# Optimization experiments

Hardware: AMD Instinct MI355X
Metric: run time of the kernel (lower is better)

The kernel has to match this reference:

```python
import jax, jax.numpy as jnp
import numpy as np

# Production-scale dims inferred from graph_construct / coord_cuda:
# coord_cuda: [batch, total_len, mat_h*mat_w, edge_num, 2]
B, T, C, H, W, K = 4, 8, 32, 40, 40, 9
EPS = 1e-8


def setup_inputs() -> dict:
    key = jax.random.key(0)
    sim_feat = jax.random.normal(key, (B, T, C, H, W), dtype=jnp.float32)
    return {"sim_feat": sim_feat}


def reference(sim_feat):
    """Motion-graph construction: similarity matrix between consecutive
    frames' node features, kNN edge selection (top edge_num), per-node
    edge weight normalization, and coordinate-displacement node init."""
    b, t, c, h, w = sim_feat.shape
    hw = h * w
    # [B, T, hw, c] node features
    feat = sim_feat.reshape(b, t, c, hw).transpose(0, 1, 3, 2)
    # cosine-style normalization for the similarity matrix
    fn = feat * jax.lax.rsqrt(jnp.sum(feat * feat, axis=-1, keepdims=True) + EPS)
    # build_similarity_matrix ('forward'): frame t nodes vs frame t+1 nodes
    # sim: [B, T-1, hw, hw] -- dominant, memory-bound intermediate
    sim = jnp.einsum('btic,btjc->btij', fn[:, :-1], fn[:, 1:])
    # build_graph_edge: top edge_num candidate edges per source node
    wgt, idx = jax.lax.top_k(sim, K)          # [B, T-1, hw, K]
    # edge_normalize: weights sum to 1 over the K edges of each node
    wgt = wgt / (jnp.sum(wgt, axis=-1, keepdims=True) + EPS)
    # target node 2D coords (y, x) via gather on flat index
    ty = idx // w
    tx = idx % w
    # source node coords (motion_node_indices analogue)
    src = jnp.arange(hw, dtype=idx.dtype)
    sy = (src // w)[None, None, :, None]
    sx = (src % w)[None, None, :, None]
    # node_init = target coord - source coord (motion displacement), [B,T-1,hw,K,2]
    node_init = jnp.stack([ty - sy, tx - sx], axis=-1)
    return wgt, idx, node_init
```

## Files before the change

kernel.cpp:

```cpp
#include <hip/hip_runtime.h>
#include <math.h>

#define BD   4
#define TD   8
#define CD   32
#define WD   40
#define KD   9
#define HWD  1600
#define TM1  7
#define NPAIR (BD * TM1)
#define OUTK ((size_t)NPAIR * HWD * KD)
#define CL   6
#define NEX  12

#define FNW_OFF   0
#define TRAW_OFF  3276800
#define RND_OFF   9830400

typedef __attribute__((ext_vector_type(8))) short short8;
typedef __attribute__((ext_vector_type(4))) float f32x4;

__device__ __forceinline__ uint f2bf(float f) {
    uint u = __float_as_uint(f);
    return (u + 0x7FFFu + ((u >> 16) & 1u)) >> 16;
}

__global__ __launch_bounds__(256)
void prep_kernel(const float* __restrict__ x, uint* __restrict__ fnw,
                 float* __restrict__ traw, double* __restrict__ rnd)
{
    const int gid  = blockIdx.x * 256 + threadIdx.x;
    const int q    = gid & 3;
    const int idx  = gid >> 2;
    const int bt   = idx / HWD;
    const int node = idx - bt * HWD;

    const float* src = x + (size_t)bt * CD * HWD + node;
    float v[8];
    float ssq = 0.f;
    double ssd = 0.0;
#pragma unroll
    for (int cc = 0; cc < 8; ++cc) {
        const float a = src[(size_t)(q * 8 + cc) * HWD];
        v[cc] = a;
        ssq += a * a;
        ssd = fma((double)a, (double)a, ssd);
    }
    ssq += __shfl_xor(ssq, 1);  ssq += __shfl_xor(ssq, 2);
    ssd += __shfl_xor(ssd, 1);  ssd += __shfl_xor(ssd, 2);

    const float rn = 1.0f / sqrtf(ssq + 1e-8f);
    if (q == 0) rnd[(size_t)bt * HWD + node] = 1.0 / sqrt(ssd + 1e-8);

    uint* dstb = fnw + (size_t)(bt * HWD + node) * 16 + q * 4;
    const uint w0 = f2bf(v[0]*rn) | (f2bf(v[1]*rn) << 16);
    const uint w1 = f2bf(v[2]*rn) | (f2bf(v[3]*rn) << 16);
    const uint w2 = f2bf(v[4]*rn) | (f2bf(v[5]*rn) << 16);
    const uint w3 = f2bf(v[6]*rn) | (f2bf(v[7]*rn) << 16);
    *(uint4*)dstb = make_uint4(w0, w1, w2, w3);

    float* dstr = traw + (size_t)(bt * HWD + node) * 32 + q * 8;
    ((float4*)dstr)[0] = make_float4(v[0], v[1], v[2], v[3]);
    ((float4*)dstr)[1] = make_float4(v[4], v[5], v[6], v[7]);
}

__global__ __launch_bounds__(256)
void topk_kernel(const uint* __restrict__ fnw, const float* __restrict__ traw,
                 const double* __restrict__ rnd, float* __restrict__ out)
{
    __shared__ uint s_ext[2][64][NEX];

    const int tid  = threadIdx.x;
    const int lane = tid & 63;
    const int wid  = tid >> 6;
    const int li   = lane & 15;
    const int gr   = lane >> 4;
    const int iq   = wid & 1;
    const int half = wid >> 1;

    const int bid  = blockIdx.x;
    const int xcd  = bid & 7;
    const int kk   = bid >> 3;
    const int work = xcd * 175 + kk;
    const int f    = work / 50;
    const int rem  = work - f * 50;
    const int b    = f / TM1;
    const int t    = f - b * TM1;
    const int bt0  = b * TD + t;
    const int bt1  = bt0 + 1;
    const int i    = rem * 32 + iq * 16 + li;

    const uint* fA = fnw + (size_t)bt0 * HWD * 16;
    const uint* fB = fnw + (size_t)bt1 * HWD * 16;

    const short8 bF = *(const short8*)(fA + (size_t)i * 16 + gr * 4);

    uint C[4][CL];
#pragma unroll
    for (int r = 0; r < 4; ++r)
#pragma unroll
        for (int k = 0; k < CL; ++k) C[r][k] = 0u;

    int jr[4];
#pragma unroll
    for (int r = 0; r < 4; ++r) jr[r] = 2047 - half * 800 - 4 * gr - r;

    const f32x4 one4 = {1.f, 1.f, 1.f, 1.f};

#define LDT(dst, s) dst = *(const short8*)(fB + (size_t)((s) * 16 + li) * 16 + gr * 4)

#define INSTILE(acc) do {                                              \
    _Pragma("unroll")                                                  \
    for (int r = 0; r < 4; ++r) {                                      \
        int ub = __float_as_int((acc)[r]);                             \
        ub = ub < 0 ? 0 : ub;                                          \
        uint u = ((uint)ub & 0xFFFFF800u) | (uint)jr[r];               \
        uint tv = u;                                                   \
        _Pragma("unroll")                                              \
        for (int k = 0; k < CL; ++k) {                                 \
            const uint lo = min(C[r][k], tv);                          \
            C[r][k] = max(C[r][k], tv);                                \
            tv = lo;                                                   \
        }                                                              \
        jr[r] -= 16;                                                   \
    }                                                                  \
} while (0)

    const int s0 = half * 50;
    short8 a0, a1, a2, a3;
    LDT(a0, s0); LDT(a1, s0 + 1); LDT(a2, s0 + 2); LDT(a3, s0 + 3);

    for (int sb = s0; sb < s0 + 44; sb += 4) {
        f32x4 acc;
        acc = __builtin_amdgcn_mfma_f32_16x16x32_bf16(a0, bF, one4, 0, 0, 0);
        LDT(a0, sb + 4);
        INSTILE(acc);
        acc = __builtin_amdgcn_mfma_f32_16x16x32_bf16(a1, bF, one4, 0, 0, 0);
        LDT(a1, sb + 5);
        INSTILE(acc);
        acc = __builtin_amdgcn_mfma_f32_16x16x32_bf16(a2, bF, one4, 0, 0, 0);
        LDT(a2, sb + 6);
        INSTILE(acc);
        acc = __builtin_amdgcn_mfma_f32_16x16x32_bf16(a3, bF, one4, 0, 0, 0);
        LDT(a3, sb + 7);
        INSTILE(acc);
    }
    {
        f32x4 acc;
        acc = __builtin_amdgcn_mfma_f32_16x16x32_bf16(a0, bF, one4, 0, 0, 0);
        LDT(a0, s0 + 48);
        INSTILE(acc);
        acc = __builtin_amdgcn_mfma_f32_16x16x32_bf16(a1, bF, one4, 0, 0, 0);
        LDT(a1, s0 + 49);
        INSTILE(acc);
        acc = __builtin_amdgcn_mfma_f32_16x16x32_bf16(a2, bF, one4, 0, 0, 0);
        INSTILE(acc);
        acc = __builtin_amdgcn_mfma_f32_16x16x32_bf16(a3, bF, one4, 0, 0, 0);
        INSTILE(acc);
        acc = __builtin_amdgcn_mfma_f32_16x16x32_bf16(a0, bF, one4, 0, 0, 0);
        INSTILE(acc);
        acc = __builtin_amdgcn_mfma_f32_16x16x32_bf16(a1, bF, one4, 0, 0, 0);
        INSTILE(acc);
    }
#undef LDT
#undef INSTILE

    uint sA[NEX];
#pragma unroll
    for (int rd = 0; rd < NEX; ++rd) {
        const uint m = max(max(C[0][0], C[1][0]), max(C[2][0], C[3][0]));
#pragma unroll
        for (int r = 0; r < 4; ++r) {
            const bool e = (C[r][0] == m);
#pragma unroll
            for (int k = 0; k < CL - 1; ++k) C[r][k] = e ? C[r][k + 1] : C[r][k];
            C[r][CL - 1] = e ? 0u : C[r][CL - 1];
        }
        sA[rd] = m;
    }

    if (half == 1) {
#pragma unroll
        for (int k = 0; k < NEX; ++k) s_ext[iq][lane][k] = sA[k];
    }
    __syncthreads();
    if (half == 1) return;

    uint sB[NEX];
#pragma unroll
    for (int q = 0; q < 3; ++q) {
        const uint4 v4 = *(const uint4*)&s_ext[iq][lane][q * 4];
        sB[q*4+0] = v4.x; sB[q*4+1] = v4.y; sB[q*4+2] = v4.z; sB[q*4+3] = v4.w;
    }

    const float* tA = traw + (size_t)bt0 * HWD * 32 + (size_t)i * 32;
    float arf[CD];
#pragma unroll
    for (int q = 0; q < 8; ++q) {
        const float4 r4 = ((const float4*)tA)[q];
        arf[4*q+0] = r4.x; arf[4*q+1] = r4.y; arf[4*q+2] = r4.z; arf[4*q+3] = r4.w;
    }
    const double rna = rnd[(size_t)bt0 * HWD + i];
    const float*  trB = traw + (size_t)bt1 * HWD * 32;
    const double* rnB = rnd + (size_t)bt1 * HWD;

    double fv[KD]; int fi[KD];
#pragma unroll
    for (int k = 0; k < KD; ++k) { fv[k] = -1.0e300; fi[k] = 0; }

    for (int rd = 0; rd < NEX; ++rd) {
        const bool tAh = sA[0] > sB[0];
        const uint m = tAh ? sA[0] : sB[0];
#pragma unroll
        for (int k = 0; k < NEX - 1; ++k) {
            sA[k] = tAh ? sA[k + 1] : sA[k];
            sB[k] = tAh ? sB[k] : sB[k + 1];
        }
        const int j = 2047 - (int)(m & 2047u);
        const float4* rb = (const float4*)(trB + (size_t)j * 32);
        double d0 = 0.0, d1 = 0.0, d2 = 0.0, d3 = 0.0;
#pragma unroll
        for (int q = 0; q < 8; ++q) {
            const float4 r4 = rb[q];
            d0 = fma((double)arf[4*q+0], (double)r4.x, d0);
            d1 = fma((double)arf[4*q+1], (double)r4.y, d1);
            d2 = fma((double)arf[4*q+2], (double)r4.z, d2);
            d3 = fma((double)arf[4*q+3], (double)r4.w, d3);
        }
        const double val = ((d0 + d1) + (d2 + d3)) * rna * rnB[j];
        if (val > fv[KD - 1]) {
            bool bg[KD];
#pragma unroll
            for (int k = 0; k < KD; ++k) bg[k] = val > fv[k];
#pragma unroll
            for (int k = KD - 1; k >= 1; --k) {
                fv[k] = bg[k - 1] ? fv[k - 1] : (bg[k] ? val : fv[k]);
                fi[k] = bg[k - 1] ? fi[k - 1] : (bg[k] ? j : fi[k]);
            }
            if (bg[0]) { fv[0] = val; fi[0] = j; }
        }
    }

    double w9v[KD]; int w9j[KD];
#pragma unroll
    for (int rd = 0; rd < KD; ++rd) {
        double hv = fv[0]; int hj = fi[0];
        {
            const double ov = __shfl_xor(hv, 16); const int oj = __shfl_xor(hj, 16);
            const bool tk = (ov > hv) || (ov == hv && oj < hj);
            hv = tk ? ov : hv; hj = tk ? oj : hj;
        }
        {
            const double ov = __shfl_xor(hv, 32); const int oj = __shfl_xor(hj, 32);
            const bool tk = (ov > hv) || (ov == hv && oj < hj);
            hv = tk ? ov : hv; hj = tk ? oj : hj;
        }
        w9v[rd] = hv; w9j[rd] = hj;
        const bool win = (fi[0] == hj);
#pragma unroll
        for (int k = 0; k < KD - 1; ++k) {
            fv[k] = win ? fv[k + 1] : fv[k];
            fi[k] = win ? fi[k + 1] : fi[k];
        }
        if (win) fv[KD - 1] = -1.0e300;
    }

    double wsum = 0.0;
#pragma unroll
    for (int k = 0; k < KD; ++k) wsum += w9v[k];
    const double winv = 1.0 / (wsum + 1e-8);

    const size_t base = ((size_t)f * HWD + i) * KD;
    const int sy = i / WD, sx = i - sy * WD;
    if (gr == 0) {
#pragma unroll
        for (int k = 0; k < KD; ++k) out[base + k] = (float)(w9v[k] * winv);
    } else if (gr == 1) {
#pragma unroll
        for (int k = 0; k < KD; ++k) out[OUTK + base + k] = (float)w9j[k];
    } else if (gr == 2) {
#pragma unroll
        for (int k = 0; k < KD; ++k) {
            const int j = w9j[k];
            out[2 * OUTK + (base + k) * 2 + 0] = (float)(j / WD - sy);
        }
    } else {
#pragma unroll
        for (int k = 0; k < KD; ++k) {
            const int j = w9j[k];
            out[2 * OUTK + (base + k) * 2 + 1] = (float)(j - (j / WD) * WD - sx);
        }
    }
}

extern "C" void kernel_launch(void* const* d_in, const int* in_sizes, int n_in,
                              void* d_out, int out_size, void* d_ws, size_t ws_size,
                              hipStream_t stream)
{
    const float* x = (const float*)d_in[0];
    uint*   fnw  = (uint*)((char*)d_ws + FNW_OFF);
    float*  traw = (float*)((char*)d_ws + TRAW_OFF);
    double* rnd  = (double*)((char*)d_ws + RND_OFF);
    float*  out  = (float*)d_out;

    prep_kernel<<<dim3((TD * BD * HWD * 4) / 256), 256, 0, stream>>>(x, fnw, traw, rnd);
    topk_kernel<<<dim3(NPAIR * 50), 256, 0, stream>>>(fnw, traw, rnd, out);
}
```

Baseline: 135.0 us.

## Split top-k kernel into scan and rerank kernels with global candidate buffer

Splits the fused MFMA scan plus exact rerank kernel into two launches. The scan kernel writes per-half candidate lists to a workspace buffer, and a separate rerank kernel reads them, so all scan waves stay busy and the barrier where half the block idled is gone. The prep kernel is reorganized so each channel quarter lives in a separate wave, with an LDS reduction instead of shuffles, and the float norm now comes from the double norm. The scan loop prefetch depth drops from four to two, which lowers register pressure. The cost is an extra launch and a global round-trip for the candidates.

```diff
diff --git a/kernel.cpp b/kernel.cpp
--- a/kernel.cpp
+++ b/kernel.cpp
@@ -16,6 +16,7 @@
 #define FNW_OFF   0
 #define TRAW_OFF  3276800
 #define RND_OFF   9830400
+#define CAND_OFF  10240000
 
 typedef __attribute__((ext_vector_type(8))) short short8;
 typedef __attribute__((ext_vector_type(4))) float f32x4;
@@ -29,28 +30,30 @@
 void prep_kernel(const float* __restrict__ x, uint* __restrict__ fnw,
                  float* __restrict__ traw, double* __restrict__ rnd)
 {
-    const int gid  = blockIdx.x * 256 + threadIdx.x;
-    const int q    = gid & 3;
-    const int idx  = gid >> 2;
-    const int bt   = idx / HWD;
-    const int node = idx - bt * HWD;
+    __shared__ double s_ssd[4][64];
+
+    const int tid = threadIdx.x;
+    const int q   = tid >> 6;
+    const int l   = tid & 63;
+    const int bt  = blockIdx.x / 25;
+    const int nb  = blockIdx.x - bt * 25;
+    const int node = nb * 64 + l;
 
     const float* src = x + (size_t)bt * CD * HWD + node;
     float v[8];
-    float ssq = 0.f;
     double ssd = 0.0;
 #pragma unroll
     for (int cc = 0; cc < 8; ++cc) {
         const float a = src[(size_t)(q * 8 + cc) * HWD];
         v[cc] = a;
-        ssq += a * a;
         ssd = fma((double)a, (double)a, ssd);
     }
-    ssq += __shfl_xor(ssq, 1);  ssq += __shfl_xor(ssq, 2);
-    ssd += __shfl_xor(ssd, 1);  ssd += __shfl_xor(ssd, 2);
-
-    const float rn = 1.0f / sqrtf(ssq + 1e-8f);
-    if (q == 0) rnd[(size_t)bt * HWD + node] = 1.0 / sqrt(ssd + 1e-8);
+    s_ssd[q][l] = ssd;
+    __syncthreads();
+    const double tot = s_ssd[0][l] + s_ssd[1][l] + s_ssd[2][l] + s_ssd[3][l];
+    const double rv  = 1.0 / sqrt(tot + 1e-8);
+    if (q == 0) rnd[(size_t)bt * HWD + node] = rv;
+    const float rn = (float)rv;
 
     uint* dstb = fnw + (size_t)(bt * HWD + node) * 16 + q * 4;
     const uint w0 = f2bf(v[0]*rn) | (f2bf(v[1]*rn) << 16);
@@ -65,11 +68,8 @@
 }
 
 __global__ __launch_bounds__(256)
-void topk_kernel(const uint* __restrict__ fnw, const float* __restrict__ traw,
-                 const double* __restrict__ rnd, float* __restrict__ out)
+void scan_kernel(const uint* __restrict__ fnw, uint* __restrict__ cand)
 {
-    __shared__ uint s_ext[2][64][NEX];
-
     const int tid  = threadIdx.x;
     const int lane = tid & 63;
     const int wid  = tid >> 6;
@@ -86,12 +86,10 @@
     const int rem  = work - f * 50;
     const int b    = f / TM1;
     const int t    = f - b * TM1;
-    const int bt0  = b * TD + t;
-    const int bt1  = bt0 + 1;
     const int i    = rem * 32 + iq * 16 + li;
 
-    const uint* fA = fnw + (size_t)bt0 * HWD * 16;
-    const uint* fB = fnw + (size_t)bt1 * HWD * 16;
+    const uint* fA = fnw + (size_t)(b * TD + t)     * HWD * 16;
+    const uint* fB = fnw + (size_t)(b * TD + t + 1) * HWD * 16;
 
     const short8 bF = *(const short8*)(fA + (size_t)i * 16 + gr * 4);
 
@@ -127,22 +125,16 @@
 } while (0)
 
     const int s0 = half * 50;
-    short8 a0, a1, a2, a3;
-    LDT(a0, s0); LDT(a1, s0 + 1); LDT(a2, s0 + 2); LDT(a3, s0 + 3);
-
-    for (int sb = s0; sb < s0 + 44; sb += 4) {
+    short8 a0, a1;
+    LDT(a0, s0); LDT(a1, s0 + 1);
+
+    for (int sb = s0; sb < s0 + 46; sb += 2) {
         f32x4 acc;
         acc = __builtin_amdgcn_mfma_f32_16x16x32_bf16(a0, bF, one4, 0, 0, 0);
-        LDT(a0, sb + 4);
+        LDT(a0, sb + 2);
         INSTILE(acc);
         acc = __builtin_amdgcn_mfma_f32_16x16x32_bf16(a1, bF, one4, 0, 0, 0);
-        LDT(a1, sb + 5);
-        INSTILE(acc);
-        acc = __builtin_amdgcn_mfma_f32_16x16x32_bf16(a2, bF, one4, 0, 0, 0);
-        LDT(a2, sb + 6);
-        INSTILE(acc);
-        acc = __builtin_amdgcn_mfma_f32_16x16x32_bf16(a3, bF, one4, 0, 0, 0);
-        LDT(a3, sb + 7);
+        LDT(a1, sb + 3);
         INSTILE(acc);
     }
     {
@@ -153,10 +145,6 @@
         acc = __builtin_amdgcn_mfma_f32_16x16x32_bf16(a1, bF, one4, 0, 0, 0);
         LDT(a1, s0 + 49);
         INSTILE(acc);
-        acc = __builtin_amdgcn_mfma_f32_16x16x32_bf16(a2, bF, one4, 0, 0, 0);
-        INSTILE(acc);
-        acc = __builtin_amdgcn_mfma_f32_16x16x32_bf16(a3, bF, one4, 0, 0, 0);
-        INSTILE(acc);
         acc = __builtin_amdgcn_mfma_f32_16x16x32_bf16(a0, bF, one4, 0, 0, 0);
         INSTILE(acc);
         acc = __builtin_amdgcn_mfma_f32_16x16x32_bf16(a1, bF, one4, 0, 0, 0);
@@ -165,7 +153,7 @@
 #undef LDT
 #undef INSTILE
 
-    uint sA[NEX];
+    uint* cp = cand + (((size_t)f * HWD + i) * 8 + gr * 2 + half) * NEX;
 #pragma unroll
     for (int rd = 0; rd < NEX; ++rd) {
         const uint m = max(max(C[0][0], C[1][0]), max(C[2][0], C[3][0]));
@@ -176,21 +164,36 @@
             for (int k = 0; k < CL - 1; ++k) C[r][k] = e ? C[r][k + 1] : C[r][k];
             C[r][CL - 1] = e ? 0u : C[r][CL - 1];
         }
-        sA[rd] = m;
-    }
-
-    if (half == 1) {
-#pragma unroll
-        for (int k = 0; k < NEX; ++k) s_ext[iq][lane][k] = sA[k];
-    }
-    __syncthreads();
-    if (half == 1) return;
-
-    uint sB[NEX];
+        cp[rd] = m;
+    }
+}
+
+__global__ __launch_bounds__(256)
+void rerank_kernel(const float* __restrict__ traw, const double* __restrict__ rnd,
+                   const uint* __restrict__ cand, float* __restrict__ out)
+{
+    const int tid  = threadIdx.x;
+    const int lane = tid & 63;
+    const int wid  = tid >> 6;
+    const int li   = lane & 15;
+    const int gr   = lane >> 4;
+    const int bid  = blockIdx.x;
+    const int f    = bid / 25;
+    const int ib   = bid - f * 25;
+    const int b    = f / TM1;
+    const int t    = f - b * TM1;
+    const int bt0  = b * TD + t;
+    const int bt1  = bt0 + 1;
+    const int i    = ib * 64 + wid * 16 + li;
+
+    const uint* cp = cand + (((size_t)f * HWD + i) * 8 + gr * 2) * NEX;
+    uint sA[NEX], sB[NEX];
 #pragma unroll
     for (int q = 0; q < 3; ++q) {
-        const uint4 v4 = *(const uint4*)&s_ext[iq][lane][q * 4];
-        sB[q*4+0] = v4.x; sB[q*4+1] = v4.y; sB[q*4+2] = v4.z; sB[q*4+3] = v4.w;
+        const uint4 va = *(const uint4*)(cp + q * 4);
+        sA[q*4+0] = va.x; sA[q*4+1] = va.y; sA[q*4+2] = va.z; sA[q*4+3] = va.w;
+        const uint4 vb = *(const uint4*)(cp + NEX + q * 4);
+        sB[q*4+0] = vb.x; sB[q*4+1] = vb.y; sB[q*4+2] = vb.z; sB[q*4+3] = vb.w;
     }
 
     const float* tA = traw + (size_t)bt0 * HWD * 32 + (size_t)i * 32;
@@ -301,8 +304,10 @@
     uint*   fnw  = (uint*)((char*)d_ws + FNW_OFF);
     float*  traw = (float*)((char*)d_ws + TRAW_OFF);
     double* rnd  = (double*)((char*)d_ws + RND_OFF);
+    uint*   cand = (uint*)((char*)d_ws + CAND_OFF);
     float*  out  = (float*)d_out;
 
-    prep_kernel<<<dim3((TD * BD * HWD * 4) / 256), 256, 0, stream>>>(x, fnw, traw, rnd);
-    topk_kernel<<<dim3(NPAIR * 50), 256, 0, stream>>>(fnw, traw, rnd, out);
-}
+    prep_kernel<<<dim3(BD * TD * 25), 256, 0, stream>>>(x, fnw, traw, rnd);
+    scan_kernel<<<dim3(NPAIR * 50), 256, 0, stream>>>(fnw, cand);
+    rerank_kernel<<<dim3(NPAIR * 25), 256, 0, stream>>>(traw, rnd, cand, out);
+}
```

Result: slower. 156.5 us (+15.9%).
